# Performance work log

Measured on AMD Instinct MI355X. Metric: run time of the kernel, lower is better.

The kernel has to match this reference:

```python
import jax, jax.numpy as jnp
import numpy as np

N_IN = 100_000
N_OUT = 400_000
K = 27          # 3^3 kernel offsets
C_IN = 64
C_OUT = 32


def setup_inputs() -> dict:
    key = jax.random.key(0)
    k1, k2, k3, k4 = jax.random.split(key, 4)
    feats = jax.random.normal(k1, (N_IN, C_IN), dtype=jnp.float32)
    # Minkowski-style weight: one [C_in, C_out] matrix per kernel offset
    weight = jax.random.normal(k2, (K, C_IN, C_OUT), dtype=jnp.float32) * (1.0 / np.sqrt(C_IN))
    # kernel maps: for each offset, M=N_IN (in_idx, out_idx) pairs
    in_map = jax.random.randint(k3, (K, N_IN), 0, N_IN, dtype=jnp.int64)
    out_map = jax.random.randint(k4, (K, N_IN), 0, N_OUT, dtype=jnp.int64)
    return {"feats": feats, "weight": weight, "in_map": in_map,
            "out_map": out_map, "n_out": N_OUT}


def reference(feats, weight, in_map, out_map, n_out):
    # gather-GEMM-scatter, vectorized over the K kernel offsets
    gathered = feats[in_map]                          # [K, M, C_in]
    msgs = jnp.einsum('kmc,kcd->kmd', gathered, weight)  # [K, M, C_out]
    out = jnp.zeros((n_out, msgs.shape[-1]), dtype=feats.dtype)
    out = out.at[out_map.reshape(-1)].add(msgs.reshape(-1, msgs.shape[-1]))
    return out
```

## Files before the change

### kernel.cpp

```cpp
#include <hip/hip_runtime.h>
#include <hip/hip_bf16.h>
#include <hip/hip_fp16.h>


using short8  = __attribute__((ext_vector_type(8))) short;
using floatx4 = __attribute__((ext_vector_type(4))) float;

constexpr int KOFF = 27;
constexpr int NIN  = 100000;
constexpr int NOUT = 400000;
constexpr int CIN  = 64;
constexpr int COUT = 32;
constexpr int MSGS = NIN;
constexpr int TILES = MSGS / 16;
constexpr int WPB   = 4;
constexpr int BLK_PER_K = 64;
constexpr int WSTRIDE = BLK_PER_K * WPB;

constexpr size_t ACC_BYTES   = (size_t)NOUT * COUT * 2;
constexpr size_t FEATS_BYTES = (size_t)NIN * CIN * 2;

constexpr int CVT_BLOCKS  = (NIN * CIN / 8) / 256;
constexpr int ZERO_BLOCKS = (int)(ACC_BYTES / 16) / 256;

__device__ __forceinline__ short f2bf(float f) {
    union { float f; unsigned u; } v; v.f = f;
    unsigned r = v.u + 0x7fff + ((v.u >> 16) & 1u);
    return (short)(r >> 16);
}

__global__ __launch_bounds__(256) void prep_kernel(
    const float* __restrict__ f, ushort* __restrict__ b, float4* __restrict__ accz)
{
    if (blockIdx.x < CVT_BLOCKS) {
        const int t = blockIdx.x * 256 + threadIdx.x;
        const float4* p = (const float4*)(f + (size_t)t * 8);
        float4 lo = p[0], hi = p[1];
        short8 v;
        v[0]=f2bf(lo.x); v[1]=f2bf(lo.y); v[2]=f2bf(lo.z); v[3]=f2bf(lo.w);
        v[4]=f2bf(hi.x); v[5]=f2bf(hi.y); v[6]=f2bf(hi.z); v[7]=f2bf(hi.w);
        *(short8*)(b + (size_t)t * 8) = v;
    } else {
        const int t = (blockIdx.x - CVT_BLOCKS) * 256 + threadIdx.x;
        accz[t] = make_float4(0.f, 0.f, 0.f, 0.f);
    }
}

__global__ __launch_bounds__(256) void spconv_pipe_kernel(
    const ushort* __restrict__ feats_bf,
    const float*  __restrict__ weight,
    const int*    __restrict__ in_map,
    const int*    __restrict__ out_map,
    __half2*      __restrict__ accum)
{
    const int k    = blockIdx.y;
    const int wave = threadIdx.x >> 6;
    const int lane = threadIdx.x & 63;
    const int col  = lane & 15;
    const int quad = lane >> 4;
    const long long kM = (long long)k * MSGS;

    const float* Wk = weight + k * (CIN * COUT);
    short8 bfr[2][2];
    #pragma unroll
    for (int s = 0; s < 2; ++s)
        #pragma unroll
        for (int t = 0; t < 2; ++t)
            #pragma unroll
            for (int j = 0; j < 8; ++j)
                bfr[s][t][j] = f2bf(Wk[(s * 32 + quad * 8 + j) * COUT + 2 * col + t]);

    #define LOAD_MAPS(t, inr, orow)                                   \
        {                                                             \
            const int tt = ((t) < TILES) ? (t) : (TILES - 1);         \
            const long long mb = kM + (long long)tt * 16;             \
            inr = in_map[mb + col];                                   \
            _Pragma("unroll")                                         \
            for (int i = 0; i < 4; ++i) orow[i] = out_map[mb + quad * 4 + i]; \
        }

    #define LOAD_FEATS(inr, a0, a1)                                   \
        {                                                             \
            const ushort* ar = feats_bf + (long long)(inr) * CIN;     \
            a0 = *(const short8*)(ar + quad * 8);                     \
            a1 = *(const short8*)(ar + 32 + quad * 8);                \
        }

    const int t0 = blockIdx.x * WPB + wave;

    int inrA, orowA[4];  LOAD_MAPS(t0,            inrA, orowA);
    int inrB, orowB[4];  LOAD_MAPS(t0 + WSTRIDE,  inrB, orowB);
    short8 a0A, a1A;     LOAD_FEATS(inrA, a0A, a1A);

    for (int t = t0; t < TILES; t += WSTRIDE) {
        int inrC, orowC[4];
        LOAD_MAPS(t + 2 * WSTRIDE, inrC, orowC);
        short8 a0B, a1B;
        LOAD_FEATS(inrB, a0B, a1B);

        floatx4 acc0 = {0.f, 0.f, 0.f, 0.f};
        floatx4 acc1 = {0.f, 0.f, 0.f, 0.f};
        acc0 = __builtin_amdgcn_mfma_f32_16x16x32_bf16(a0A, bfr[0][0], acc0, 0, 0, 0);
        acc1 = __builtin_amdgcn_mfma_f32_16x16x32_bf16(a0A, bfr[0][1], acc1, 0, 0, 0);
        acc0 = __builtin_amdgcn_mfma_f32_16x16x32_bf16(a1A, bfr[1][0], acc0, 0, 0, 0);
        acc1 = __builtin_amdgcn_mfma_f32_16x16x32_bf16(a1A, bfr[1][1], acc1, 0, 0, 0);

        #pragma unroll
        for (int i = 0; i < 4; ++i) {
            __half2 h = __floats2half2_rn(acc0[i], acc1[i]);
            unsafeAtomicAdd(accum + (long long)orowA[i] * 16 + col, h);
        }

        inrA = inrB; a0A = a0B; a1A = a1B;
        inrB = inrC;
        #pragma unroll
        for (int i = 0; i < 4; ++i) { orowA[i] = orowB[i]; orowB[i] = orowC[i]; }
    }
    #undef LOAD_MAPS
    #undef LOAD_FEATS
}

__global__ __launch_bounds__(256) void spconv_fp16acc_f32feats_kernel(
    const float*  __restrict__ feats_f32,
    const float*  __restrict__ weight,
    const int*    __restrict__ in_map,
    const int*    __restrict__ out_map,
    __half2*      __restrict__ accum)
{
    const int k    = blockIdx.y;
    const int wave = threadIdx.x >> 6;
    const int lane = threadIdx.x & 63;
    const int col  = lane & 15;
    const int quad = lane >> 4;
    const int tile = blockIdx.x * WPB + wave;
    if (tile >= TILES) return;
    const int m0 = tile * 16;
    const long long mapbase = (long long)k * MSGS;

    const int in_row = in_map[mapbase + m0 + col];
    int orow[4];
    #pragma unroll
    for (int i = 0; i < 4; ++i) orow[i] = out_map[mapbase + m0 + quad * 4 + i];

    const float* Wk = weight + k * (CIN * COUT);
    short8 bfr[2][2];
    #pragma unroll
    for (int s = 0; s < 2; ++s)
        #pragma unroll
        for (int t = 0; t < 2; ++t)
            #pragma unroll
            for (int j = 0; j < 8; ++j)
                bfr[s][t][j] = f2bf(Wk[(s * 32 + quad * 8 + j) * COUT + 2 * col + t]);

    const float* ar = feats_f32 + (long long)in_row * CIN + quad * 8;
    const float4* p0 = (const float4*)ar;
    const float4* p1 = (const float4*)(ar + 32);
    float4 l0 = p0[0], h0 = p0[1], l1 = p1[0], h1 = p1[1];
    short8 a0, a1;
    a0[0]=f2bf(l0.x); a0[1]=f2bf(l0.y); a0[2]=f2bf(l0.z); a0[3]=f2bf(l0.w);
    a0[4]=f2bf(h0.x); a0[5]=f2bf(h0.y); a0[6]=f2bf(h0.z); a0[7]=f2bf(h0.w);
    a1[0]=f2bf(l1.x); a1[1]=f2bf(l1.y); a1[2]=f2bf(l1.z); a1[3]=f2bf(l1.w);
    a1[4]=f2bf(h1.x); a1[5]=f2bf(h1.y); a1[6]=f2bf(h1.z); a1[7]=f2bf(h1.w);

    floatx4 acc0 = {0.f, 0.f, 0.f, 0.f};
    floatx4 acc1 = {0.f, 0.f, 0.f, 0.f};
    acc0 = __builtin_amdgcn_mfma_f32_16x16x32_bf16(a0, bfr[0][0], acc0, 0, 0, 0);
    acc1 = __builtin_amdgcn_mfma_f32_16x16x32_bf16(a0, bfr[0][1], acc1, 0, 0, 0);
    acc0 = __builtin_amdgcn_mfma_f32_16x16x32_bf16(a1, bfr[1][0], acc0, 0, 0, 0);
    acc1 = __builtin_amdgcn_mfma_f32_16x16x32_bf16(a1, bfr[1][1], acc1, 0, 0, 0);

    #pragma unroll
    for (int i = 0; i < 4; ++i) {
        __half2 h = __floats2half2_rn(acc0[i], acc1[i]);
        unsafeAtomicAdd(accum + (long long)orow[i] * 16 + col, h);
    }
}

__global__ __launch_bounds__(256) void spconv_f32atomic_kernel(
    const float* __restrict__ feats,
    const float* __restrict__ weight,
    const int*   __restrict__ in_map,
    const int*   __restrict__ out_map,
    float*       __restrict__ out)
{
    const int k    = blockIdx.y;
    const int wave = threadIdx.x >> 6;
    const int lane = threadIdx.x & 63;
    const int col  = lane & 15;
    const int quad = lane >> 4;
    const int tile = blockIdx.x * WPB + wave;
    if (tile >= TILES) return;
    const int m0 = tile * 16;
    const long long mapbase = (long long)k * MSGS;

    const float* Wk = weight + k * (CIN * COUT);
    short8 bfr[2][2];
    #pragma unroll
    for (int s = 0; s < 2; ++s)
        #pragma unroll
        for (int t = 0; t < 2; ++t)
            #pragma unroll
            for (int j = 0; j < 8; ++j)
                bfr[s][t][j] = f2bf(Wk[(s * 32 + quad * 8 + j) * COUT + t * 16 + col]);

    const int in_row = in_map[mapbase + m0 + col];
    const float* arow = feats + (long long)in_row * CIN + quad * 8;

    floatx4 acc0 = {0.f, 0.f, 0.f, 0.f};
    floatx4 acc1 = {0.f, 0.f, 0.f, 0.f};
    #pragma unroll
    for (int s = 0; s < 2; ++s) {
        const float4* p = (const float4*)(arow + s * 32);
        float4 lo = p[0], hi = p[1];
        short8 a;
        a[0]=f2bf(lo.x); a[1]=f2bf(lo.y); a[2]=f2bf(lo.z); a[3]=f2bf(lo.w);
        a[4]=f2bf(hi.x); a[5]=f2bf(hi.y); a[6]=f2bf(hi.z); a[7]=f2bf(hi.w);
        acc0 = __builtin_amdgcn_mfma_f32_16x16x32_bf16(a, bfr[s][0], acc0, 0, 0, 0);
        acc1 = __builtin_amdgcn_mfma_f32_16x16x32_bf16(a, bfr[s][1], acc1, 0, 0, 0);
    }
    #pragma unroll
    for (int i = 0; i < 4; ++i) {
        const int orow = out_map[mapbase + m0 + quad * 4 + i];
        float* po = out + (long long)orow * COUT;
        atomicAdd(po + col,      acc0[i]);
        atomicAdd(po + col + 16, acc1[i]);
    }
}

__global__ __launch_bounds__(256) void h2_to_f32_kernel(
    const __half2* __restrict__ acc, float* __restrict__ out)
{
    const int t = blockIdx.x * blockDim.x + threadIdx.x;
    const __half2* p = acc + (size_t)t * 4;
    float2 f0 = __half22float2(p[0]);
    float2 f1 = __half22float2(p[1]);
    float2 f2 = __half22float2(p[2]);
    float2 f3 = __half22float2(p[3]);
    float4* o = (float4*)out + (size_t)t * 2;
    o[0] = make_float4(f0.x, f0.y, f1.x, f1.y);
    o[1] = make_float4(f2.x, f2.y, f3.x, f3.y);
}

extern "C" void kernel_launch(void* const* d_in, const int* in_sizes, int n_in,
                              void* d_out, int out_size, void* d_ws, size_t ws_size,
                              hipStream_t stream) {
    const float* feats   = (const float*)d_in[0];
    const float* weight  = (const float*)d_in[1];
    const int*   in_map  = (const int*)d_in[2];
    const int*   out_map = (const int*)d_in[3];
    float*       out     = (float*)d_out;

    if (ws_size >= ACC_BYTES + FEATS_BYTES) {
        __half2* accum    = (__half2*)d_ws;
        ushort*  feats_bf = (ushort*)((char*)d_ws + ACC_BYTES);

        prep_kernel<<<CVT_BLOCKS + ZERO_BLOCKS, 256, 0, stream>>>(
            feats, feats_bf, (float4*)accum);
        spconv_pipe_kernel<<<dim3(BLK_PER_K, KOFF), 256, 0, stream>>>(
            feats_bf, weight, in_map, out_map, accum);
        h2_to_f32_kernel<<<(NOUT * 16 / 4) / 256, 256, 0, stream>>>(accum, out);
    } else if (ws_size >= ACC_BYTES) {
        __half2* accum = (__half2*)d_ws;
        hipMemsetAsync(accum, 0, ACC_BYTES, stream);
        spconv_fp16acc_f32feats_kernel<<<dim3((TILES + WPB - 1) / WPB, KOFF), 256, 0, stream>>>(
            feats, weight, in_map, out_map, accum);
        h2_to_f32_kernel<<<(NOUT * 16 / 4) / 256, 256, 0, stream>>>(accum, out);
    } else {
        hipMemsetAsync(d_out, 0, (size_t)out_size * sizeof(float), stream);
        spconv_f32atomic_kernel<<<dim3((TILES + WPB - 1) / WPB, KOFF), 256, 0, stream>>>(
            feats, weight, in_map, out_map, out);
    }
}
```

Before: 260.1 us.

## Replace atomic scatter with binned message buffer and shared-memory segmented reduction

Adds a new default path when the workspace is large enough. A fill kernel buckets every (offset, message) pair by output slice of 256 rows, using shared-memory histograms and global counters. A msgs kernel writes the fp16 GEMM results densely to a buffer, and a reduce kernel accumulates each slice in fp32 shared memory before writing the output directly. The aim is to remove global fp16 atomics and the separate zero and convert passes. In exchange it writes and reads a large intermediate message buffer, and silently drops entries if any bucket exceeds its fixed capacity (CAP_S, CAPG).

Measured after the change: 349.4 us. +34.3%, slower.

```diff
diff --git a/kernel.cpp b/kernel.cpp
--- a/kernel.cpp
+++ b/kernel.cpp
@@ -11,14 +11,33 @@
 constexpr int NOUT = 400000;
 constexpr int CIN  = 64;
 constexpr int COUT = 32;
-constexpr int MSGS = NIN;
+constexpr int MSGS = 100000;
+constexpr int TOTAL_MSGS = KOFF * MSGS;
 constexpr int TILES = MSGS / 16;
 constexpr int WPB   = 4;
 constexpr int BLK_PER_K = 64;
 constexpr int WSTRIDE = BLK_PER_K * WPB;
 
-constexpr size_t ACC_BYTES   = (size_t)NOUT * COUT * 2;
-constexpr size_t FEATS_BYTES = (size_t)NIN * CIN * 2;
+constexpr int SL_ROWS = 256;
+constexpr int NS      = (NOUT + SL_ROWS - 1) / SL_ROWS;
+constexpr int CAP_S   = 2048;
+constexpr int CAPG    = 384;
+
+constexpr int FILL_BLOCKS = 512;
+constexpr int MPB = (TOTAL_MSGS + FILL_BLOCKS - 1) / FILL_BLOCKS;
+constexpr int FILL_ITERS = (MPB + 1023) / 1024;
+
+constexpr size_t FEATS_BYTES  = (size_t)NIN * CIN * 2;
+constexpr size_t MSGS_BYTES   = (size_t)TOTAL_MSGS * COUT * 2;
+constexpr size_t SLISTS_BYTES = (size_t)NS * CAP_S * 4;
+constexpr size_t GCNT_BYTES   = 8192;
+constexpr size_t OFF_MSGS   = FEATS_BYTES;
+constexpr size_t OFF_SLISTS = OFF_MSGS + MSGS_BYTES;
+constexpr size_t OFF_GCNT   = OFF_SLISTS + ((SLISTS_BYTES + 255) & ~(size_t)255);
+constexpr size_t WS_NEED1   = OFF_GCNT + GCNT_BYTES;
+
+constexpr size_t ACC_BYTES = (size_t)NOUT * COUT * 2;
+constexpr size_t WS_NEED2  = ACC_BYTES + FEATS_BYTES;
 
 constexpr int CVT_BLOCKS  = (NIN * CIN / 8) / 256;
 constexpr int ZERO_BLOCKS = (int)(ACC_BYTES / 16) / 256;
@@ -29,7 +48,217 @@
     return (short)(r >> 16);
 }
 
-__global__ __launch_bounds__(256) void prep_kernel(
+__global__ __launch_bounds__(256) void feats_cvt_kernel(
+    const float* __restrict__ f, ushort* __restrict__ b)
+{
+    const int t = blockIdx.x * 256 + threadIdx.x;
+    const float4* p = (const float4*)(f + (size_t)t * 8);
+    float4 lo = p[0], hi = p[1];
+    short8 v;
+    v[0]=f2bf(lo.x); v[1]=f2bf(lo.y); v[2]=f2bf(lo.z); v[3]=f2bf(lo.w);
+    v[4]=f2bf(hi.x); v[5]=f2bf(hi.y); v[6]=f2bf(hi.z); v[7]=f2bf(hi.w);
+    *(short8*)(b + (size_t)t * 8) = v;
+}
+
+__global__ __launch_bounds__(1024) void fill_kernel(
+    const int* __restrict__ out_map,
+    int* __restrict__ slists,
+    int* __restrict__ gcnt)
+{
+    const int tid  = threadIdx.x;
+    const int base = blockIdx.x * MPB;
+
+    __shared__ int hist[NS];
+    __shared__ int hbase[NS];
+    for (int ss = tid; ss < NS; ss += 1024) hist[ss] = 0;
+    __syncthreads();
+
+    #pragma unroll 1
+    for (int it = 0; it < FILL_ITERS; ++it) {
+        const int off = it * 1024 + tid;
+        const int m = base + off;
+        if (off < MPB && m < TOTAL_MSGS)
+            atomicAdd(&hist[out_map[m] >> 8], 1);
+    }
+    __syncthreads();
+    for (int ss = tid; ss < NS; ss += 1024) {
+        const int h = hist[ss];
+        hbase[ss] = h ? atomicAdd(&gcnt[ss], h) : 0;
+        hist[ss] = 0;
+    }
+    __syncthreads();
+    #pragma unroll 1
+    for (int it = 0; it < FILL_ITERS; ++it) {
+        const int off = it * 1024 + tid;
+        const int m = base + off;
+        if (off < MPB && m < TOTAL_MSGS) {
+            const int orow = out_map[m];
+            const int ss   = orow >> 8;
+            const int pos  = hbase[ss] + atomicAdd(&hist[ss], 1);
+            if (pos < CAP_S)
+                slists[(size_t)ss * CAP_S + pos] = (m << 8) | (orow & 255);
+        }
+    }
+}
+
+__global__ __launch_bounds__(256) void msgs_kernel(
+    const ushort* __restrict__ feats_bf,
+    const float*  __restrict__ weight,
+    const int*    __restrict__ in_map,
+    __half2*      __restrict__ msgs_h2)
+{
+    const int k    = blockIdx.y;
+    const int wave = threadIdx.x >> 6;
+    const int lane = threadIdx.x & 63;
+    const int col  = lane & 15;
+    const int quad = lane >> 4;
+    const long long kM = (long long)k * MSGS;
+
+    const float* Wk = weight + k * (CIN * COUT);
+    short8 bfr[2][2];
+    #pragma unroll
+    for (int s = 0; s < 2; ++s)
+        #pragma unroll
+        for (int t = 0; t < 2; ++t)
+            #pragma unroll
+            for (int j = 0; j < 8; ++j)
+                bfr[s][t][j] = f2bf(Wk[(s * 32 + quad * 8 + j) * COUT + 2 * col + t]);
+
+    #define LOAD_INR(t, inr)                                          \
+        {                                                             \
+            const int tt = ((t) < TILES) ? (t) : (TILES - 1);         \
+            inr = in_map[kM + (long long)tt * 16 + col];              \
+        }
+    #define LOAD_FEATS(inr, a0, a1)                                   \
+        {                                                             \
+            const ushort* ar = feats_bf + (long long)(inr) * CIN;     \
+            a0 = *(const short8*)(ar + quad * 8);                     \
+            a1 = *(const short8*)(ar + 32 + quad * 8);                \
+        }
+
+    const int t0 = blockIdx.x * WPB + wave;
+    int inrA, inrB;
+    LOAD_INR(t0, inrA);
+    LOAD_INR(t0 + WSTRIDE, inrB);
+    short8 a0A, a1A;
+    LOAD_FEATS(inrA, a0A, a1A);
+
+    for (int t = t0; t < TILES; t += WSTRIDE) {
+        int inrC;
+        LOAD_INR(t + 2 * WSTRIDE, inrC);
+        short8 a0B, a1B;
+        LOAD_FEATS(inrB, a0B, a1B);
+
+        floatx4 c0 = {0.f, 0.f, 0.f, 0.f};
+        floatx4 c1 = {0.f, 0.f, 0.f, 0.f};
+        c0 = __builtin_amdgcn_mfma_f32_16x16x32_bf16(a0A, bfr[0][0], c0, 0, 0, 0);
+        c1 = __builtin_amdgcn_mfma_f32_16x16x32_bf16(a0A, bfr[0][1], c1, 0, 0, 0);
+        c0 = __builtin_amdgcn_mfma_f32_16x16x32_bf16(a1A, bfr[1][0], c0, 0, 0, 0);
+        c1 = __builtin_amdgcn_mfma_f32_16x16x32_bf16(a1A, bfr[1][1], c1, 0, 0, 0);
+
+        const size_t mb = (size_t)(kM + (long long)t * 16);
+        #pragma unroll
+        for (int i = 0; i < 4; ++i)
+            msgs_h2[(mb + quad * 4 + i) * 16 + col] = __floats2half2_rn(c0[i], c1[i]);
+
+        inrA = inrB; a0A = a0B; a1A = a1B;
+        inrB = inrC;
+    }
+    #undef LOAD_INR
+    #undef LOAD_FEATS
+}
+
+__global__ __launch_bounds__(512) void reduce_kernel(
+    const unsigned int* __restrict__ msgs_u32,
+    const int* __restrict__ slists,
+    const int* __restrict__ gcnt,
+    float* __restrict__ out)
+{
+    const int s    = blockIdx.x;
+    const int tid  = threadIdx.x;
+    const int wave = tid >> 6;
+    const int lane = tid & 63;
+
+    __shared__ float acc[SL_ROWS * COUT];
+    __shared__ int   binned[8 * CAPG];
+    __shared__ int   bcnt[8];
+
+    {
+        float4* av = (float4*)acc;
+        for (int i = tid; i < SL_ROWS * COUT / 4; i += 512)
+            av[i] = make_float4(0.f, 0.f, 0.f, 0.f);
+        if (tid < 8) bcnt[tid] = 0;
+    }
+    __syncthreads();
+
+    const int cnt_s = min(gcnt[s], CAP_S);
+    const int* sl = slists + (size_t)s * CAP_S;
+
+    for (int idx = tid; idx < cnt_s; idx += 512) {
+        const int e = sl[idx];
+        const int g = (e >> 5) & 7;
+        #pragma unroll
+        for (int gi = 0; gi < 8; ++gi) {
+            const unsigned long long m = __ballot(g == gi);
+            if (m == 0) continue;
+            const int leader = __ffsll((unsigned long long)m) - 1;
+            int base = 0;
+            if (lane == leader) base = atomicAdd(&bcnt[gi], __popcll(m));
+            base = __shfl(base, leader);
+            if (g == gi) {
+                const int pos = base + __popcll(m & ((1ull << lane) - 1));
+                if (pos < CAPG) binned[gi * CAPG + pos] = e;
+            }
+        }
+    }
+    __syncthreads();
+
+    {
+        const int g   = wave;
+        const int cnt = min(bcnt[g], CAPG);
+        const int* bg = binned + g * CAPG;
+        const int sub = lane >> 4;
+        const int cl  = lane & 15;
+
+        int  e1 = -1, e2 = -1;
+        unsigned int u1 = 0, u2 = 0;
+        if (sub < cnt)     e1 = bg[sub];
+        if (4 + sub < cnt) e2 = bg[4 + sub];
+        if (e1 >= 0) u1 = msgs_u32[(size_t)(e1 >> 8) * 16 + cl];
+        if (e2 >= 0) u2 = msgs_u32[(size_t)(e2 >> 8) * 16 + cl];
+
+        #pragma unroll 1
+        for (int i = 0; i < cnt; i += 4) {
+            int e3 = -1; unsigned int u3 = 0;
+            if (i + 8 + sub < cnt) e3 = bg[i + 8 + sub];
+            if (e3 >= 0) u3 = msgs_u32[(size_t)(e3 >> 8) * 16 + cl];
+
+            #pragma unroll
+            for (int j = 0; j < 4; ++j) {
+                if (sub == j && e1 >= 0) {
+                    const int lr = e1 & 255;
+                    const float2 f = __half22float2(*(const __half2*)&u1);
+                    float2* p = (float2*)(acc + lr * COUT + cl * 2);
+                    float2 d = *p;
+                    d.x += f.x; d.y += f.y;
+                    *p = d;
+                }
+            }
+            e1 = e2; u1 = u2; e2 = e3; u2 = u3;
+        }
+    }
+    __syncthreads();
+
+    const int rowbase = s * SL_ROWS;
+    const int rows = min(SL_ROWS, NOUT - rowbase);
+    for (int idx = tid; idx < rows * 8; idx += 512) {
+        const int r = idx >> 3, q = idx & 7;
+        *((float4*)(out + (size_t)(rowbase + r) * COUT) + q) =
+            *(const float4*)(acc + r * COUT + q * 4);
+    }
+}
+
+__global__ __launch_bounds__(256) void prep4_kernel(
     const float* __restrict__ f, ushort* __restrict__ b, float4* __restrict__ accz)
 {
     if (blockIdx.x < CVT_BLOCKS) {
@@ -78,7 +307,6 @@
             _Pragma("unroll")                                         \
             for (int i = 0; i < 4; ++i) orow[i] = out_map[mb + quad * 4 + i]; \
         }
-
     #define LOAD_FEATS(inr, a0, a1)                                   \
         {                                                             \
             const ushort* ar = feats_bf + (long long)(inr) * CIN;     \
@@ -87,9 +315,8 @@
         }
 
     const int t0 = blockIdx.x * WPB + wave;
-
-    int inrA, orowA[4];  LOAD_MAPS(t0,            inrA, orowA);
-    int inrB, orowB[4];  LOAD_MAPS(t0 + WSTRIDE,  inrB, orowB);
+    int inrA, orowA[4];  LOAD_MAPS(t0,           inrA, orowA);
+    int inrB, orowB[4];  LOAD_MAPS(t0 + WSTRIDE, inrB, orowB);
     short8 a0A, a1A;     LOAD_FEATS(inrA, a0A, a1A);
 
     for (int t = t0; t < TILES; t += WSTRIDE) {
@@ -98,19 +325,18 @@
         short8 a0B, a1B;
         LOAD_FEATS(inrB, a0B, a1B);
 
-        floatx4 acc0 = {0.f, 0.f, 0.f, 0.f};
-        floatx4 acc1 = {0.f, 0.f, 0.f, 0.f};
-        acc0 = __builtin_amdgcn_mfma_f32_16x16x32_bf16(a0A, bfr[0][0], acc0, 0, 0, 0);
-        acc1 = __builtin_amdgcn_mfma_f32_16x16x32_bf16(a0A, bfr[0][1], acc1, 0, 0, 0);
-        acc0 = __builtin_amdgcn_mfma_f32_16x16x32_bf16(a1A, bfr[1][0], acc0, 0, 0, 0);
-        acc1 = __builtin_amdgcn_mfma_f32_16x16x32_bf16(a1A, bfr[1][1], acc1, 0, 0, 0);
+        floatx4 c0 = {0.f, 0.f, 0.f, 0.f};
+        floatx4 c1 = {0.f, 0.f, 0.f, 0.f};
+        c0 = __builtin_amdgcn_mfma_f32_16x16x32_bf16(a0A, bfr[0][0], c0, 0, 0, 0);
+        c1 = __builtin_amdgcn_mfma_f32_16x16x32_bf16(a0A, bfr[0][1], c1, 0, 0, 0);
+        c0 = __builtin_amdgcn_mfma_f32_16x16x32_bf16(a1A, bfr[1][0], c0, 0, 0, 0);
+        c1 = __builtin_amdgcn_mfma_f32_16x16x32_bf16(a1A, bfr[1][1], c1, 0, 0, 0);
 
         #pragma unroll
         for (int i = 0; i < 4; ++i) {
-            __half2 h = __floats2half2_rn(acc0[i], acc1[i]);
+            __half2 h = __floats2half2_rn(c0[i], c1[i]);
             unsafeAtomicAdd(accum + (long long)orowA[i] * 16 + col, h);
         }
-
         inrA = inrB; a0A = a0B; a1A = a1B;
         inrB = inrC;
         #pragma unroll
@@ -120,12 +346,26 @@
     #undef LOAD_FEATS
 }
 
-__global__ __launch_bounds__(256) void spconv_fp16acc_f32feats_kernel(
-    const float*  __restrict__ feats_f32,
-    const float*  __restrict__ weight,
-    const int*    __restrict__ in_map,
-    const int*    __restrict__ out_map,
-    __half2*      __restrict__ accum)
+__global__ __launch_bounds__(256) void h2_to_f32_kernel(
+    const __half2* __restrict__ acc, float* __restrict__ out)
+{
+    const int t = blockIdx.x * blockDim.x + threadIdx.x;
+    const __half2* p = acc + (size_t)t * 4;
+    float2 f0 = __half22float2(p[0]);
+    float2 f1 = __half22float2(p[1]);
+    float2 f2 = __half22float2(p[2]);
+    float2 f3 = __half22float2(p[3]);
+    float4* o = (float4*)out + (size_t)t * 2;
+    o[0] = make_float4(f0.x, f0.y, f1.x, f1.y);
+    o[1] = make_float4(f2.x, f2.y, f3.x, f3.y);
+}
+
+__global__ __launch_bounds__(256) void spconv_f32atomic_kernel(
+    const float* __restrict__ feats,
+    const float* __restrict__ weight,
+    const int*   __restrict__ in_map,
+    const int*   __restrict__ out_map,
+    float*       __restrict__ out)
 {
     const int k    = blockIdx.y;
     const int wave = threadIdx.x >> 6;
@@ -137,108 +377,38 @@
     const int m0 = tile * 16;
     const long long mapbase = (long long)k * MSGS;
 
-    const int in_row = in_map[mapbase + m0 + col];
-    int orow[4];
-    #pragma unroll
-    for (int i = 0; i < 4; ++i) orow[i] = out_map[mapbase + m0 + quad * 4 + i];
-
     const float* Wk = weight + k * (CIN * COUT);
     short8 bfr[2][2];
     #pragma unroll
-    for (int s = 0; s < 2; ++s)
+    for (int ss = 0; ss < 2; ++ss)
         #pragma unroll
         for (int t = 0; t < 2; ++t)
             #pragma unroll
             for (int j = 0; j < 8; ++j)
-                bfr[s][t][j] = f2bf(Wk[(s * 32 + quad * 8 + j) * COUT + 2 * col + t]);
-
-    const float* ar = feats_f32 + (long long)in_row * CIN + quad * 8;
-    const float4* p0 = (const float4*)ar;
-    const float4* p1 = (const float4*)(ar + 32);
-    float4 l0 = p0[0], h0 = p0[1], l1 = p1[0], h1 = p1[1];
-    short8 a0, a1;
-    a0[0]=f2bf(l0.x); a0[1]=f2bf(l0.y); a0[2]=f2bf(l0.z); a0[3]=f2bf(l0.w);
-    a0[4]=f2bf(h0.x); a0[5]=f2bf(h0.y); a0[6]=f2bf(h0.z); a0[7]=f2bf(h0.w);
-    a1[0]=f2bf(l1.x); a1[1]=f2bf(l1.y); a1[2]=f2bf(l1.z); a1[3]=f2bf(l1.w);
-    a1[4]=f2bf(h1.x); a1[5]=f2bf(h1.y); a1[6]=f2bf(h1.z); a1[7]=f2bf(h1.w);
-
-    floatx4 acc0 = {0.f, 0.f, 0.f, 0.f};
-    floatx4 acc1 = {0.f, 0.f, 0.f, 0.f};
-    acc0 = __builtin_amdgcn_mfma_f32_16x16x32_bf16(a0, bfr[0][0], acc0, 0, 0, 0);
-    acc1 = __builtin_amdgcn_mfma_f32_16x16x32_bf16(a0, bfr[0][1], acc1, 0, 0, 0);
-    acc0 = __builtin_amdgcn_mfma_f32_16x16x32_bf16(a1, bfr[1][0], acc0, 0, 0, 0);
-    acc1 = __builtin_amdgcn_mfma_f32_16x16x32_bf16(a1, bfr[1][1], acc1, 0, 0, 0);
-
-    #pragma unroll
-    for (int i = 0; i < 4; ++i) {
-        __half2 h = __floats2half2_rn(acc0[i], acc1[i]);
-        unsafeAtomicAdd(accum + (long long)orow[i] * 16 + col, h);
-    }
-}
-
-__global__ __launch_bounds__(256) void spconv_f32atomic_kernel(
-    const float* __restrict__ feats,
-    const float* __restrict__ weight,
-    const int*   __restrict__ in_map,
-    const int*   __restrict__ out_map,
-    float*       __restrict__ out)
-{
-    const int k    = blockIdx.y;
-    const int wave = threadIdx.x >> 6;
-    const int lane = threadIdx.x & 63;
-    const int col  = lane & 15;
-    const int quad = lane >> 4;
-    const int tile = blockIdx.x * WPB + wave;
-    if (tile >= TILES) return;
-    const int m0 = tile * 16;
-    const long long mapbase = (long long)k * MSGS;
-
-    const float* Wk = weight + k * (CIN * COUT);
-    short8 bfr[2][2];
-    #pragma unroll
-    for (int s = 0; s < 2; ++s)
-        #pragma unroll
-        for (int t = 0; t < 2; ++t)
-            #pragma unroll
-            for (int j = 0; j < 8; ++j)
-                bfr[s][t][j] = f2bf(Wk[(s * 32 + quad * 8 + j) * COUT + t * 16 + col]);
+                bfr[ss][t][j] = f2bf(Wk[(ss * 32 + quad * 8 + j) * COUT + t * 16 + col]);
 
     const int in_row = in_map[mapbase + m0 + col];
     const float* arow = feats + (long long)in_row * CIN + quad * 8;
 
-    floatx4 acc0 = {0.f, 0.f, 0.f, 0.f};
-    floatx4 acc1 = {0.f, 0.f, 0.f, 0.f};
+    floatx4 c0 = {0.f, 0.f, 0.f, 0.f};
+    floatx4 c1 = {0.f, 0.f, 0.f, 0.f};
     #pragma unroll
-    for (int s = 0; s < 2; ++s) {
-        const float4* p = (const float4*)(arow + s * 32);
+    for (int ss = 0; ss < 2; ++ss) {
+        const float4* p = (const float4*)(arow + ss * 32);
         float4 lo = p[0], hi = p[1];
         short8 a;
         a[0]=f2bf(lo.x); a[1]=f2bf(lo.y); a[2]=f2bf(lo.z); a[3]=f2bf(lo.w);
         a[4]=f2bf(hi.x); a[5]=f2bf(hi.y); a[6]=f2bf(hi.z); a[7]=f2bf(hi.w);
-        acc0 = __builtin_amdgcn_mfma_f32_16x16x32_bf16(a, bfr[s][0], acc0, 0, 0, 0);
-        acc1 = __builtin_amdgcn_mfma_f32_16x16x32_bf16(a, bfr[s][1], acc1, 0, 0, 0);
+        c0 = __builtin_amdgcn_mfma_f32_16x16x32_bf16(a, bfr[ss][0], c0, 0, 0, 0);
+        c1 = __builtin_amdgcn_mfma_f32_16x16x32_bf16(a, bfr[ss][1], c1, 0, 0, 0);
     }
     #pragma unroll
     for (int i = 0; i < 4; ++i) {
         const int orow = out_map[mapbase + m0 + quad * 4 + i];
         float* po = out + (long long)orow * COUT;
-        atomicAdd(po + col,      acc0[i]);
-        atomicAdd(po + col + 16, acc1[i]);
-    }
-}
-
-__global__ __launch_bounds__(256) void h2_to_f32_kernel(
-    const __half2* __restrict__ acc, float* __restrict__ out)
-{
-    const int t = blockIdx.x * blockDim.x + threadIdx.x;
-    const __half2* p = acc + (size_t)t * 4;
-    float2 f0 = __half22float2(p[0]);
-    float2 f1 = __half22float2(p[1]);
-    float2 f2 = __half22float2(p[2]);
-    float2 f3 = __half22float2(p[3]);
-    float4* o = (float4*)out + (size_t)t * 2;
-    o[0] = make_float4(f0.x, f0.y, f1.x, f1.y);
-    o[1] = make_float4(f2.x, f2.y, f3.x, f3.y);
+        atomicAdd(po + col,      c0[i]);
+        atomicAdd(po + col + 16, c1[i]);
+    }
 }
 
 extern "C" void kernel_launch(void* const* d_in, const int* in_sizes, int n_in,
@@ -250,20 +420,26 @@
     const int*   out_map = (const int*)d_in[3];
     float*       out     = (float*)d_out;
 
-    if (ws_size >= ACC_BYTES + FEATS_BYTES) {
+    if (ws_size >= WS_NEED1) {
+        ushort*       feats_bf = (ushort*)d_ws;
+        __half2*      msgs     = (__half2*)((char*)d_ws + OFF_MSGS);
+        int*          slists   = (int*)((char*)d_ws + OFF_SLISTS);
+        int*          gcnt     = (int*)((char*)d_ws + OFF_GCNT);
+
+        hipMemsetAsync(gcnt, 0, GCNT_BYTES, stream);
+        feats_cvt_kernel<<<CVT_BLOCKS, 256, 0, stream>>>(feats, feats_bf);
+        fill_kernel<<<FILL_BLOCKS, 1024, 0, stream>>>(out_map, slists, gcnt);
+        msgs_kernel<<<dim3(BLK_PER_K, KOFF), 256, 0, stream>>>(
+            feats_bf, weight, in_map, msgs);
+        reduce_kernel<<<NS, 512, 0, stream>>>(
+            (const unsigned int*)msgs, slists, gcnt, out);
+    } else if (ws_size >= WS_NEED2) {
         __half2* accum    = (__half2*)d_ws;
         ushort*  feats_bf = (ushort*)((char*)d_ws + ACC_BYTES);
-
-        prep_kernel<<<CVT_BLOCKS + ZERO_BLOCKS, 256, 0, stream>>>(
+        prep4_kernel<<<CVT_BLOCKS + ZERO_BLOCKS, 256, 0, stream>>>(
             feats, feats_bf, (float4*)accum);
         spconv_pipe_kernel<<<dim3(BLK_PER_K, KOFF), 256, 0, stream>>>(
             feats_bf, weight, in_map, out_map, accum);
-        h2_to_f32_kernel<<<(NOUT * 16 / 4) / 256, 256, 0, stream>>>(accum, out);
-    } else if (ws_size >= ACC_BYTES) {
-        __half2* accum = (__half2*)d_ws;
-        hipMemsetAsync(accum, 0, ACC_BYTES, stream);
-        spconv_fp16acc_f32feats_kernel<<<dim3((TILES + WPB - 1) / WPB, KOFF), 256, 0, stream>>>(
-            feats, weight, in_map, out_map, accum);
         h2_to_f32_kernel<<<(NOUT * 16 / 4) / 256, 256, 0, stream>>>(accum, out);
     } else {
         hipMemsetAsync(d_out, 0, (size_t)out_size * sizeof(float), stream);
```
